# Kernel tuning notes

Hardware: AMD Instinct MI355X
Metric: run time of the kernel (lower is better)

The kernel has to match this reference:

```python
import jax, jax.numpy as jnp
import numpy as np

B, T, D, H, R = 64, 128, 128, 128, 4  # num_T == num_H == num_D forced by shape consistency
E = D * R  # SwiGLU expansion dim
EPS = 1e-5


def _pswiglu(x, Wu, bu, Wg, bg, Wd, bd):
    # x: [B,T,D]; per-token independent SwiGLU MLPs batched as one einsum
    up = jnp.einsum('btd,tde->bte', x, Wu) + bu          # [B,T,E]
    gate = jax.nn.silu(jnp.einsum('btd,tde->bte', x, Wg) + bg)
    return jnp.einsum('bte,ted->btd', up * gate, Wd) + bd  # [B,T,D]


def _rmsnorm(x, scale):
    rms = jnp.sqrt(jnp.mean(x * x, axis=-1, keepdims=True) + EPS)
    return x / rms * scale


def _token_mix(x, nT, nD, nH):
    # reshape (B,nT,nD)->(B,nT,nH,dk), transpose, merge -> (B,nH,nT*dk)
    dk = nD // nH
    b = x.shape[0]
    return x.reshape(b, nT, nH, dk).transpose(0, 2, 1, 3).reshape(b, nH, nT * dk)


def setup_inputs() -> dict:
    key = jax.random.key(0)
    ks = jax.random.split(key, 7)
    s = 0.02
    return {
        'x': jax.random.normal(ks[0], (B, T, D), dtype=jnp.float32),
        'W1_up': jax.random.normal(ks[1], (T, D, E), dtype=jnp.float32) * s,
        'b1_up': jnp.zeros((T, E), jnp.float32),
        'W1_gate': jax.random.normal(ks[2], (T, D, E), dtype=jnp.float32) * s,
        'b1_gate': jnp.zeros((T, E), jnp.float32),
        'W1_down': jax.random.normal(ks[3], (T, E, D), dtype=jnp.float32) * s,
        'b1_down': jnp.zeros((T, D), jnp.float32),
        'scale1': jnp.ones((D,), jnp.float32),
        'W2_up': jax.random.normal(ks[4], (T, D, E), dtype=jnp.float32) * s,
        'b2_up': jnp.zeros((T, E), jnp.float32),
        'W2_gate': jax.random.normal(ks[5], (T, D, E), dtype=jnp.float32) * s,
        'b2_gate': jnp.zeros((T, E), jnp.float32),
        'W2_down': jax.random.normal(ks[6], (T, E, D), dtype=jnp.float32) * s,
        'b2_down': jnp.zeros((T, D), jnp.float32),
        'scale2': jnp.ones((D,), jnp.float32),
    }


def reference(x, W1_up, b1_up, W1_gate, b1_gate, W1_down, b1_down, scale1,
              W2_up, b2_up, W2_gate, b2_gate, W2_down, b2_down, scale2):
    mixed = _token_mix(x, T, D, H)                         # [B,H,T*D/H] == [B,N,N]
    x1 = _rmsnorm(mixed + _pswiglu(mixed, W1_up, b1_up, W1_gate, b1_gate, W1_down, b1_down), scale1)
    rev = _token_mix(x1, T, H, D)                          # revert transpose
    out = _rmsnorm(rev + _pswiglu(rev, W2_up, b2_up, W2_gate, b2_gate, W2_down, b2_down), scale2)
    return out
```

## Files before the change

### kernel.cpp

```cpp
#include <hip/hip_runtime.h>

typedef __bf16 bf16x8 __attribute__((ext_vector_type(8)));
typedef float f32x4 __attribute__((ext_vector_type(4)));
typedef unsigned int uint;

union Frag { __bf16 b[8]; bf16x8 v; unsigned short u[8]; };

__device__ __forceinline__ unsigned short bfbits(float f) {
  union { __bf16 h; unsigned short s; } c; c.h = (__bf16)f; return c.s;
}
__device__ __forceinline__ float bf2f(unsigned short h) {
  return __uint_as_float(((uint)h) << 16);
}

#define BAR() asm volatile("s_waitcnt lgkmcnt(0)\n\ts_barrier" ::: "memory")

template <typename T>
__global__ __launch_bounds__(256) void transpose_in(const T* __restrict__ src,
                                                    unsigned short* __restrict__ dst) {
  __shared__ unsigned short tile[64][68];
  const int b  = blockIdx.x >> 2;
  const int f0 = ((blockIdx.x >> 1) & 1) * 64;
  const int s0 = (blockIdx.x & 1) * 64;
  const int j = threadIdx.x & 63, i0 = threadIdx.x >> 6;
  const T* sp = src + b * 16384 + f0 * 128 + s0 + j;
#pragma unroll
  for (int p = 0; p < 16; ++p) {
    const int i = i0 + p * 4;
    if constexpr (sizeof(T) == 4) tile[i][j] = bfbits((float)sp[i * 128]);
    else                          tile[i][j] = (unsigned short)sp[i * 128];
  }
  __syncthreads();
  unsigned short* dp = dst + s0 * 8192 + b * 128 + f0 + j;
#pragma unroll
  for (int p = 0; p < 16; ++p) {
    const int i = i0 + p * 4;
    dp[(size_t)i * 8192] = tile[j][i];
  }
}

__global__ __launch_bounds__(512, 4) void mlp_main(
    const unsigned short* __restrict__ Xt,
    const float* __restrict__ Wu, const float* __restrict__ bu,
    const float* __restrict__ Wg, const float* __restrict__ bg,
    const float* __restrict__ Wd,
    unsigned short* __restrict__ partial)
{
  const int bid = blockIdx.x;
  const int s = bid >> 2, q = bid & 3;
  const int tid = threadIdx.x;
  const int wv = tid >> 6, lane = tid & 63;
  const int l16 = lane & 15, lg = lane >> 4;
  const int col = wv * 16 + l16;

  __shared__ __align__(16) unsigned short xa[64 * 136];

  const float* WuS = Wu + (size_t)s * 65536 + q * 128;
  const float* WgS = Wg + (size_t)s * 65536 + q * 128;
  const float* WdS = Wd + (size_t)s * 65536 + (size_t)q * 16384;

  const float* pu = WuS + (size_t)(lg * 8) * 512 + col;
  const float* pg = WgS + (size_t)(lg * 8) * 512 + col;
  const float* pd = WdS + (size_t)(lg * 8) * 128 + col;

  float ub[2][8], gb[2][8], db[2][8];
#pragma unroll
  for (int j = 0; j < 8; ++j) { ub[0][j] = pu[(size_t)j * 512]; gb[0][j] = pg[(size_t)j * 512]; }
  const float buv = bu[s * 512 + q * 128 + col];
  const float bgv = bg[s * 512 + q * 128 + col];

#pragma unroll
  for (int cc = 0; cc < 2; ++cc) {
    const int c = tid * 2 + cc;
    const int m = c >> 4, ch = c & 15;
    uint4 v = *(const uint4*)(Xt + (size_t)s * 8192 + m * 128 + ch * 8);
    *(uint4*)&xa[m * 136 + ((ch ^ (m & 7)) << 3)] = v;
  }
  BAR();

  Frag a[4];
  f32x4 au[4] = {}, ag[4] = {};
#pragma unroll
  for (int kk = 0; kk < 4; ++kk) {
    if (kk < 3) {
#pragma unroll
      for (int j = 0; j < 8; ++j) {
        ub[(kk + 1) & 1][j] = pu[(size_t)((kk + 1) * 32 + j) * 512];
        gb[(kk + 1) & 1][j] = pg[(size_t)((kk + 1) * 32 + j) * 512];
      }
    }
#pragma unroll
    for (int mt = 0; mt < 4; ++mt) {
      const int m = mt * 16 + l16;
      a[mt].v = *(const bf16x8*)&xa[m * 136 + (((kk * 4 + lg) ^ (m & 7)) << 3)];
    }
    Frag fu, fg;
#pragma unroll
    for (int j = 0; j < 8; ++j) {
      fu.b[j] = (__bf16)ub[kk & 1][j];
      fg.b[j] = (__bf16)gb[kk & 1][j];
    }
#pragma unroll
    for (int mt = 0; mt < 4; ++mt) {
      au[mt] = __builtin_amdgcn_mfma_f32_16x16x32_bf16(a[mt].v, fu.v, au[mt], 0, 0, 0);
      ag[mt] = __builtin_amdgcn_mfma_f32_16x16x32_bf16(a[mt].v, fg.v, ag[mt], 0, 0, 0);
    }
  }

#pragma unroll
  for (int j = 0; j < 8; ++j) db[0][j] = pd[(size_t)j * 128];

  float a2v[4][4];
#pragma unroll
  for (int mt = 0; mt < 4; ++mt)
#pragma unroll
    for (int r = 0; r < 4; ++r) {
      const float uv = au[mt][r] + buv;
      const float gv = ag[mt][r] + bgv;
      a2v[mt][r] = uv * (gv / (1.f + __expf(-gv)));
    }

  BAR();
#pragma unroll
  for (int mt = 0; mt < 4; ++mt)
#pragma unroll
    for (int r = 0; r < 4; ++r) {
      const int m = mt * 16 + lg * 4 + r;
      xa[m * 136 + (((col >> 3) ^ (m & 7)) << 3) + (col & 7)] = bfbits(a2v[mt][r]);
    }
  BAR();

  f32x4 ad[4] = {};
#pragma unroll
  for (int kk = 0; kk < 4; ++kk) {
    if (kk < 3) {
#pragma unroll
      for (int j = 0; j < 8; ++j)
        db[(kk + 1) & 1][j] = pd[(size_t)((kk + 1) * 32 + j) * 128];
    }
#pragma unroll
    for (int mt = 0; mt < 4; ++mt) {
      const int m = mt * 16 + l16;
      a[mt].v = *(const bf16x8*)&xa[m * 136 + (((kk * 4 + lg) ^ (m & 7)) << 3)];
    }
    Frag fd;
#pragma unroll
    for (int j = 0; j < 8; ++j) fd.b[j] = (__bf16)db[kk & 1][j];
#pragma unroll
    for (int mt = 0; mt < 4; ++mt)
      ad[mt] = __builtin_amdgcn_mfma_f32_16x16x32_bf16(a[mt].v, fd.v, ad[mt], 0, 0, 0);
  }

  unsigned short* po = partial + (size_t)bid * 8192;
#pragma unroll
  for (int mt = 0; mt < 4; ++mt)
#pragma unroll
    for (int r = 0; r < 4; ++r)
      po[(mt * 16 + lg * 4 + r) * 128 + col] = bfbits(ad[mt][r]);
}

template <typename TO>
__global__ __launch_bounds__(256) void finish(
    const unsigned short* __restrict__ part, const unsigned short* __restrict__ xt,
    const float* __restrict__ bd, const float* __restrict__ scale,
    TO* __restrict__ y)
{
  const int s = blockIdx.x >> 1, half = blockIdx.x & 1;
  const int wvt = threadIdx.x >> 6, lane = threadIdx.x & 63;
  const int d0 = lane * 2;
  const float sc0 = scale[d0], sc1 = scale[d0 + 1];
  const float b0 = bd[s * 128 + d0], b1 = bd[s * 128 + d0 + 1];
  const unsigned short* pb = part + (size_t)s * 4 * 8192;
  const unsigned short* xb = xt + (size_t)s * 8192;
  for (int i = 0; i < 8; ++i) {
    const int b = half * 32 + i * 4 + wvt;
    const uint rx = *(const uint*)(xb + b * 128 + d0);
    float z0 = b0 + bf2f((unsigned short)rx);
    float z1 = b1 + bf2f((unsigned short)(rx >> 16));
#pragma unroll
    for (int p = 0; p < 4; ++p) {
      const uint rp = *(const uint*)(pb + p * 8192 + b * 128 + d0);
      z0 += bf2f((unsigned short)rp);
      z1 += bf2f((unsigned short)(rp >> 16));
    }
    float ss = z0 * z0 + z1 * z1;
#pragma unroll
    for (int off = 32; off; off >>= 1) ss += __shfl_xor(ss, off);
    const float inv = rsqrtf(ss * (1.f / 128.f) + 1e-5f);
    if constexpr (sizeof(TO) == 4) {
      float2 o = make_float2(z0 * inv * sc0, z1 * inv * sc1);
      *(float2*)((float*)y + (size_t)b * 16384 + s * 128 + d0) = o;
    } else {
      const uint o = (uint)bfbits(z0 * inv * sc0) | ((uint)bfbits(z1 * inv * sc1) << 16);
      *(uint*)((unsigned short*)y + (size_t)b * 16384 + s * 128 + d0) = o;
    }
  }
}

extern "C" void kernel_launch(void* const* d_in, const int* in_sizes, int n_in,
                              void* d_out, int out_size, void* d_ws, size_t ws_size,
                              hipStream_t stream) {
  (void)in_sizes; (void)n_in; (void)out_size; (void)ws_size;
  const float* x   = (const float*)d_in[0];
  const float* W1u = (const float*)d_in[1];
  const float* b1u = (const float*)d_in[2];
  const float* W1g = (const float*)d_in[3];
  const float* b1g = (const float*)d_in[4];
  const float* W1d = (const float*)d_in[5];
  const float* b1d = (const float*)d_in[6];
  const float* sc1 = (const float*)d_in[7];
  const float* W2u = (const float*)d_in[8];
  const float* b2u = (const float*)d_in[9];
  const float* W2g = (const float*)d_in[10];
  const float* b2g = (const float*)d_in[11];
  const float* W2d = (const float*)d_in[12];
  const float* b2d = (const float*)d_in[13];
  const float* sc2 = (const float*)d_in[14];
  float* out = (float*)d_out;

  unsigned short* xt   = (unsigned short*)d_ws;
  unsigned short* y1   = xt + (size_t)1048576;
  unsigned short* part = y1 + (size_t)1048576;

  transpose_in<float><<<256, 256, 0, stream>>>(x, xt);
  mlp_main<<<512, 512, 0, stream>>>(xt, W1u, b1u, W1g, b1g, W1d, part);
  finish<unsigned short><<<256, 256, 0, stream>>>(part, xt, b1d, sc1, y1);
  transpose_in<unsigned short><<<256, 256, 0, stream>>>(y1, xt);
  mlp_main<<<512, 512, 0, stream>>>(xt, W2u, b2u, W2g, b2g, W2d, part);
  finish<float><<<256, 256, 0, stream>>>(part, xt, b2d, sc2, out);
}
```

Measured before the change: 60.65 us.

## Stream weight tiles into LDS via async global_load_lds with triple buffering

Replaces per-thread register prefetch of fp32 weight columns with asynchronous global-to-LDS loads (global_load_lds) into a three-slot LDS ring buffer, keeping two weight tiles in flight while MFMAs consume the third. Barriers wait on vmcnt so loads overlap compute. The down-projection weights are prefetched during the gate/up phase. The activation tile drops its XOR swizzle in favour of a padded stride, and weight tiles get a column swizzle instead. This adds LDS use (about 48KB plus the activation tile), which may limit occupancy at 4 blocks per CU. It also adds more barriers.

```diff
diff --git a/kernel.cpp b/kernel.cpp
--- a/kernel.cpp
+++ b/kernel.cpp
@@ -4,6 +4,8 @@
 typedef float f32x4 __attribute__((ext_vector_type(4)));
 typedef unsigned int uint;
 
+#define XA_STR 152
+
 union Frag { __bf16 b[8]; bf16x8 v; unsigned short u[8]; };
 
 __device__ __forceinline__ unsigned short bfbits(float f) {
@@ -13,7 +15,8 @@
   return __uint_as_float(((uint)h) << 16);
 }
 
-#define BAR() asm volatile("s_waitcnt lgkmcnt(0)\n\ts_barrier" ::: "memory")
+#define WAIT_BAR(N) asm volatile("s_waitcnt vmcnt(" #N ") lgkmcnt(0)\n\ts_barrier" ::: "memory")
+#define LGKM_BAR()  asm volatile("s_waitcnt lgkmcnt(0)\n\ts_barrier" ::: "memory")
 
 template <typename T>
 __global__ __launch_bounds__(256) void transpose_in(const T* __restrict__ src,
@@ -53,62 +56,92 @@
   const int l16 = lane & 15, lg = lane >> 4;
   const int col = wv * 16 + l16;
 
-  __shared__ __align__(16) unsigned short xa[64 * 136];
+  __shared__ __align__(16) float wb[3][4096];
+  __shared__ __align__(16) unsigned short xa[64 * XA_STR];
 
   const float* WuS = Wu + (size_t)s * 65536 + q * 128;
   const float* WgS = Wg + (size_t)s * 65536 + q * 128;
   const float* WdS = Wd + (size_t)s * 65536 + (size_t)q * 16384;
 
-  const float* pu = WuS + (size_t)(lg * 8) * 512 + col;
-  const float* pg = WgS + (size_t)(lg * 8) * 512 + col;
-  const float* pd = WdS + (size_t)(lg * 8) * 128 + col;
-
-  float ub[2][8], gb[2][8], db[2][8];
-#pragma unroll
-  for (int j = 0; j < 8; ++j) { ub[0][j] = pu[(size_t)j * 512]; gb[0][j] = pg[(size_t)j * 512]; }
+  auto ISSUE = [&](const float* base, int rs, float* bb) {
+#pragma unroll
+    for (int r = 0; r < 2; ++r) {
+      const int p = (r << 9) + tid;
+      const int k = p >> 5, ch = p & 31;
+      const int chs = ch ^ (((k >> 3) & 1) << 2);
+      __builtin_amdgcn_global_load_lds(
+          (const __attribute__((address_space(1))) void*)(base + (size_t)k * rs + (chs << 2)),
+          (__attribute__((address_space(3))) void*)(bb + (p << 2)), 16, 0, 0);
+    }
+  };
+
+  Frag a[4];
+  auto LOADA = [&](int kk) {
+#pragma unroll
+    for (int mt = 0; mt < 4; ++mt)
+      a[mt].v = *(const bf16x8*)&xa[(mt * 16 + l16) * XA_STR + ((kk * 4 + lg) << 3)];
+  };
+
+  const int cswz = col ^ ((lg & 1) << 4);
+  auto BFRAG = [&](const float* bb) {
+    Frag f;
+    const float* bp = bb + (lg << 3) * 128 + cswz;
+#pragma unroll
+    for (int j = 0; j < 8; ++j) f.b[j] = (__bf16)bp[j * 128];
+    return f;
+  };
+
+  f32x4 au[4] = {}, ag[4] = {}, ad[4] = {};
+  auto MFMA4 = [&](const Frag& f, f32x4* acc) {
+#pragma unroll
+    for (int mt = 0; mt < 4; ++mt)
+      acc[mt] = __builtin_amdgcn_mfma_f32_16x16x32_bf16(a[mt].v, f.v, acc[mt], 0, 0, 0);
+  };
+
+  uint4 xv[2];
+#pragma unroll
+  for (int cc = 0; cc < 2; ++cc) {
+    const int p = (cc << 9) + tid;
+    const int m = p >> 4, ch = p & 15;
+    xv[cc] = *(const uint4*)(Xt + (size_t)s * 8192 + m * 128 + (ch << 3));
+  }
   const float buv = bu[s * 512 + q * 128 + col];
   const float bgv = bg[s * 512 + q * 128 + col];
-
+  __builtin_amdgcn_sched_barrier(0);
+  ISSUE(WuS, 512, wb[0]);
+  ISSUE(WgS, 512, wb[1]);
+  __builtin_amdgcn_sched_barrier(0);
 #pragma unroll
   for (int cc = 0; cc < 2; ++cc) {
-    const int c = tid * 2 + cc;
-    const int m = c >> 4, ch = c & 15;
-    uint4 v = *(const uint4*)(Xt + (size_t)s * 8192 + m * 128 + ch * 8);
-    *(uint4*)&xa[m * 136 + ((ch ^ (m & 7)) << 3)] = v;
-  }
-  BAR();
-
-  Frag a[4];
-  f32x4 au[4] = {}, ag[4] = {};
-#pragma unroll
-  for (int kk = 0; kk < 4; ++kk) {
-    if (kk < 3) {
-#pragma unroll
-      for (int j = 0; j < 8; ++j) {
-        ub[(kk + 1) & 1][j] = pu[(size_t)((kk + 1) * 32 + j) * 512];
-        gb[(kk + 1) & 1][j] = pg[(size_t)((kk + 1) * 32 + j) * 512];
-      }
-    }
-#pragma unroll
-    for (int mt = 0; mt < 4; ++mt) {
-      const int m = mt * 16 + l16;
-      a[mt].v = *(const bf16x8*)&xa[m * 136 + (((kk * 4 + lg) ^ (m & 7)) << 3)];
-    }
-    Frag fu, fg;
-#pragma unroll
-    for (int j = 0; j < 8; ++j) {
-      fu.b[j] = (__bf16)ub[kk & 1][j];
-      fg.b[j] = (__bf16)gb[kk & 1][j];
-    }
-#pragma unroll
-    for (int mt = 0; mt < 4; ++mt) {
-      au[mt] = __builtin_amdgcn_mfma_f32_16x16x32_bf16(a[mt].v, fu.v, au[mt], 0, 0, 0);
-      ag[mt] = __builtin_amdgcn_mfma_f32_16x16x32_bf16(a[mt].v, fg.v, ag[mt], 0, 0, 0);
-    }
-  }
-
-#pragma unroll
-  for (int j = 0; j < 8; ++j) db[0][j] = pd[(size_t)j * 128];
+    const int p = (cc << 9) + tid;
+    const int m = p >> 4, ch = p & 15;
+    *(uint4*)&xa[m * XA_STR + (ch << 3)] = xv[cc];
+  }
+
+  WAIT_BAR(2);
+  LOADA(0); { Frag f = BFRAG(wb[0]); MFMA4(f, au); }
+  ISSUE(WuS + 32 * 512, 512, wb[2]);
+  WAIT_BAR(2);
+  { Frag f = BFRAG(wb[1]); MFMA4(f, ag); }
+  ISSUE(WgS + 32 * 512, 512, wb[0]);
+  WAIT_BAR(2);
+  LOADA(1); { Frag f = BFRAG(wb[2]); MFMA4(f, au); }
+  ISSUE(WuS + 64 * 512, 512, wb[1]);
+  WAIT_BAR(2);
+  { Frag f = BFRAG(wb[0]); MFMA4(f, ag); }
+  ISSUE(WgS + 64 * 512, 512, wb[2]);
+  WAIT_BAR(2);
+  LOADA(2); { Frag f = BFRAG(wb[1]); MFMA4(f, au); }
+  ISSUE(WuS + 96 * 512, 512, wb[0]);
+  WAIT_BAR(2);
+  { Frag f = BFRAG(wb[2]); MFMA4(f, ag); }
+  ISSUE(WgS + 96 * 512, 512, wb[1]);
+  WAIT_BAR(2);
+  LOADA(3); { Frag f = BFRAG(wb[0]); MFMA4(f, au); }
+  ISSUE(WdS, 128, wb[2]);
+  WAIT_BAR(2);
+  { Frag f = BFRAG(wb[1]); MFMA4(f, ag); }
+  ISSUE(WdS + 32 * 128, 128, wb[0]);
 
   float a2v[4][4];
 #pragma unroll
@@ -119,37 +152,23 @@
       const float gv = ag[mt][r] + bgv;
       a2v[mt][r] = uv * (gv / (1.f + __expf(-gv)));
     }
-
-  BAR();
+  LGKM_BAR();
 #pragma unroll
   for (int mt = 0; mt < 4; ++mt)
 #pragma unroll
-    for (int r = 0; r < 4; ++r) {
-      const int m = mt * 16 + lg * 4 + r;
-      xa[m * 136 + (((col >> 3) ^ (m & 7)) << 3) + (col & 7)] = bfbits(a2v[mt][r]);
-    }
-  BAR();
-
-  f32x4 ad[4] = {};
-#pragma unroll
-  for (int kk = 0; kk < 4; ++kk) {
-    if (kk < 3) {
-#pragma unroll
-      for (int j = 0; j < 8; ++j)
-        db[(kk + 1) & 1][j] = pd[(size_t)((kk + 1) * 32 + j) * 128];
-    }
-#pragma unroll
-    for (int mt = 0; mt < 4; ++mt) {
-      const int m = mt * 16 + l16;
-      a[mt].v = *(const bf16x8*)&xa[m * 136 + (((kk * 4 + lg) ^ (m & 7)) << 3)];
-    }
-    Frag fd;
-#pragma unroll
-    for (int j = 0; j < 8; ++j) fd.b[j] = (__bf16)db[kk & 1][j];
-#pragma unroll
-    for (int mt = 0; mt < 4; ++mt)
-      ad[mt] = __builtin_amdgcn_mfma_f32_16x16x32_bf16(a[mt].v, fd.v, ad[mt], 0, 0, 0);
-  }
+    for (int r = 0; r < 4; ++r)
+      xa[(mt * 16 + lg * 4 + r) * XA_STR + col] = bfbits(a2v[mt][r]);
+
+  WAIT_BAR(2);
+  LOADA(0); { Frag f = BFRAG(wb[2]); MFMA4(f, ad); }
+  ISSUE(WdS + 64 * 128, 128, wb[1]);
+  WAIT_BAR(2);
+  LOADA(1); { Frag f = BFRAG(wb[0]); MFMA4(f, ad); }
+  ISSUE(WdS + 96 * 128, 128, wb[2]);
+  WAIT_BAR(2);
+  LOADA(2); { Frag f = BFRAG(wb[1]); MFMA4(f, ad); }
+  WAIT_BAR(0);
+  LOADA(3); { Frag f = BFRAG(wb[2]); MFMA4(f, ad); }
 
   unsigned short* po = partial + (size_t)bid * 8192;
 #pragma unroll
```

Result: slower. 61.88 us (+2.0%).

## Stage weights via vectorized inline-asm loads through LDS with deep prefetch

Applied to the files above, without the earlier changes.

Replaces the per-lane scalar strided weight loads in mlp_main with coalesced global_load_dwordx4 inline-asm loads that are staged through shared memory (SU/SG) and then read back transposed into bf16 fragments. Loads for up, gate and down weights are issued several k-steps ahead and tracked with explicit vmcnt waits, so down-projection weights stream in while the up/gate MFMAs run. The activation tile drops the XOR swizzle and uses a padded stride of 152 instead. Shared memory use grows and two barriers are added per k-step, which may reduce occupancy. The hand-counted vmcnt values are fragile if the compiler reorders or adds memory operations.

```diff
diff --git a/kernel.cpp b/kernel.cpp
--- a/kernel.cpp
+++ b/kernel.cpp
@@ -4,6 +4,8 @@
 typedef float f32x4 __attribute__((ext_vector_type(4)));
 typedef unsigned int uint;
 
+#define XA_STR 152
+
 union Frag { __bf16 b[8]; bf16x8 v; unsigned short u[8]; };
 
 __device__ __forceinline__ unsigned short bfbits(float f) {
@@ -13,7 +15,14 @@
   return __uint_as_float(((uint)h) << 16);
 }
 
-#define BAR() asm volatile("s_waitcnt lgkmcnt(0)\n\ts_barrier" ::: "memory")
+#define GLOAD4(dst, voff, base) \
+  asm volatile("global_load_dwordx4 %0, %1, %2" : "=v"(dst) : "v"(voff), "s"(base))
+#define GLOAD4I(dst, voff, base, IMM) \
+  asm volatile("global_load_dwordx4 %0, %1, %2 offset:" #IMM : "=v"(dst) : "v"(voff), "s"(base))
+#define GLOAD1(dst, voff, base) \
+  asm volatile("global_load_dword %0, %1, %2" : "=v"(dst) : "v"(voff), "s"(base))
+#define WAITV(N) asm volatile("s_waitcnt vmcnt(" #N ")" ::: "memory")
+#define BARX()   asm volatile("s_waitcnt lgkmcnt(0)\n\ts_barrier" ::: "memory")
 
 template <typename T>
 __global__ __launch_bounds__(256) void transpose_in(const T* __restrict__ src,
@@ -53,62 +62,86 @@
   const int l16 = lane & 15, lg = lane >> 4;
   const int col = wv * 16 + l16;
 
-  __shared__ __align__(16) unsigned short xa[64 * 136];
+  __shared__ __align__(16) float SU[32 * 128];
+  __shared__ __align__(16) float SG[32 * 128];
+  __shared__ __align__(16) unsigned short xa[64 * XA_STR];
 
   const float* WuS = Wu + (size_t)s * 65536 + q * 128;
   const float* WgS = Wg + (size_t)s * 65536 + q * 128;
   const float* WdS = Wd + (size_t)s * 65536 + (size_t)q * 16384;
-
-  const float* pu = WuS + (size_t)(lg * 8) * 512 + col;
-  const float* pg = WgS + (size_t)(lg * 8) * 512 + col;
-  const float* pd = WdS + (size_t)(lg * 8) * 128 + col;
-
-  float ub[2][8], gb[2][8], db[2][8];
-#pragma unroll
-  for (int j = 0; j < 8; ++j) { ub[0][j] = pu[(size_t)j * 512]; gb[0][j] = pg[(size_t)j * 512]; }
-  const float buv = bu[s * 512 + q * 128 + col];
-  const float bgv = bg[s * 512 + q * 128 + col];
-
-#pragma unroll
-  for (int cc = 0; cc < 2; ++cc) {
-    const int c = tid * 2 + cc;
-    const int m = c >> 4, ch = c & 15;
-    uint4 v = *(const uint4*)(Xt + (size_t)s * 8192 + m * 128 + ch * 8);
-    *(uint4*)&xa[m * 136 + ((ch ^ (m & 7)) << 3)] = v;
-  }
-  BAR();
+  const float* buS = bu + s * 512 + q * 128;
+  const float* bgS = bg + s * 512 + q * 128;
+  const unsigned short* XtS = Xt + (size_t)s * 8192;
+
+  uint vuo = (uint)((4 * wv + 2 + (lane >> 5)) * 2048 + (lane & 31) * 16);
+  uint vdo = (uint)((4 * wv + (lane >> 5)) * 512 + (lane & 31) * 16);
+  const uint vbo = (uint)(col * 4);
+  const uint vx0 = (uint)(tid * 16), vx1 = vx0 + 8192;
+
+  f32x4 uq[3][2], gq[3][2], dq[4][2];
+  f32x4 xq0, xq1;
+  float buv, bgv;
+
+#define ISSUE_U(SET) do { \
+    GLOAD4I(uq[SET][0], vuo, WuS, -4096); GLOAD4(uq[SET][1], vuo, WuS); \
+    GLOAD4I(gq[SET][0], vuo, WgS, -4096); GLOAD4(gq[SET][1], vuo, WgS); \
+    vuo += 65536; } while (0)
+#define ISSUE_D(SET) do { \
+    GLOAD4(dq[SET][0], vdo, WdS); GLOAD4I(dq[SET][1], vdo, WdS, 1024); \
+    vdo += 16384; } while (0)
+
+  GLOAD4(xq0, vx0, XtS);
+  GLOAD4(xq1, vx1, XtS);
+  GLOAD1(buv, vbo, buS);
+  GLOAD1(bgv, vbo, bgS);
+  ISSUE_U(0); ISSUE_U(1); ISSUE_U(2);
+
+  WAITV(12);
+  {
+    const int m0 = tid >> 4, ch0 = tid & 15;
+    *(f32x4*)&xa[m0 * XA_STR + (ch0 << 3)] = xq0;
+    const int p1 = tid + 512, m1 = p1 >> 4, ch1 = p1 & 15;
+    *(f32x4*)&xa[m1 * XA_STR + (ch1 << 3)] = xq1;
+  }
+  BARX();
+
+  const int wsA = (4 * wv + (lane >> 5)) * 128 + (lane & 31) * 4;
+  const int wsB = wsA + 256;
 
   Frag a[4];
-  f32x4 au[4] = {}, ag[4] = {};
-#pragma unroll
-  for (int kk = 0; kk < 4; ++kk) {
-    if (kk < 3) {
-#pragma unroll
-      for (int j = 0; j < 8; ++j) {
-        ub[(kk + 1) & 1][j] = pu[(size_t)((kk + 1) * 32 + j) * 512];
-        gb[(kk + 1) & 1][j] = pg[(size_t)((kk + 1) * 32 + j) * 512];
-      }
-    }
-#pragma unroll
-    for (int mt = 0; mt < 4; ++mt) {
-      const int m = mt * 16 + l16;
-      a[mt].v = *(const bf16x8*)&xa[m * 136 + (((kk * 4 + lg) ^ (m & 7)) << 3)];
-    }
-    Frag fu, fg;
-#pragma unroll
-    for (int j = 0; j < 8; ++j) {
-      fu.b[j] = (__bf16)ub[kk & 1][j];
-      fg.b[j] = (__bf16)gb[kk & 1][j];
-    }
-#pragma unroll
-    for (int mt = 0; mt < 4; ++mt) {
-      au[mt] = __builtin_amdgcn_mfma_f32_16x16x32_bf16(a[mt].v, fu.v, au[mt], 0, 0, 0);
-      ag[mt] = __builtin_amdgcn_mfma_f32_16x16x32_bf16(a[mt].v, fg.v, ag[mt], 0, 0, 0);
-    }
-  }
-
-#pragma unroll
-  for (int j = 0; j < 8; ++j) db[0][j] = pd[(size_t)j * 128];
+#define LOADA(KK) do { \
+    _Pragma("unroll") \
+    for (int mt = 0; mt < 4; ++mt) \
+      a[mt].v = *(const bf16x8*)&xa[(mt * 16 + l16) * XA_STR + (((KK) * 4 + lg) << 3)]; \
+  } while (0)
+
+#define BF(f, SL) do { \
+    const float* bp = (SL) + (lg * 8) * 128 + col; \
+    _Pragma("unroll") \
+    for (int j = 0; j < 8; ++j) f.b[j] = (__bf16)bp[j * 128]; } while (0)
+
+  f32x4 au[4] = {}, ag[4] = {}, ad[4] = {};
+#define MFMA4(f, acc) do { \
+    _Pragma("unroll") \
+    for (int mt = 0; mt < 4; ++mt) \
+      acc[mt] = __builtin_amdgcn_mfma_f32_16x16x32_bf16(a[mt].v, f.v, acc[mt], 0, 0, 0); \
+  } while (0)
+
+#define UP_STEP(SET, KK, ISSUE_STMT) do { \
+    BARX();  \
+    *(f32x4*)&SU[wsA] = uq[SET][0]; *(f32x4*)&SU[wsB] = uq[SET][1]; \
+    *(f32x4*)&SG[wsA] = gq[SET][0]; *(f32x4*)&SG[wsB] = gq[SET][1]; \
+    ISSUE_STMT; \
+    BARX();  \
+    LOADA(KK); \
+    { Frag fu; BF(fu, SU); MFMA4(fu, au); } \
+    { Frag fg; BF(fg, SG); MFMA4(fg, ag); } \
+  } while (0)
+
+  WAITV(8);  UP_STEP(0, 0, ISSUE_U(0));
+  WAITV(8);  UP_STEP(1, 1, ISSUE_D(0));
+  WAITV(6);  UP_STEP(2, 2, ISSUE_D(1));
+  WAITV(4);  UP_STEP(0, 3, ISSUE_D(2));
 
   float a2v[4][4];
 #pragma unroll
@@ -119,37 +152,26 @@
       const float gv = ag[mt][r] + bgv;
       a2v[mt][r] = uv * (gv / (1.f + __expf(-gv)));
     }
-
-  BAR();
+  BARX();
 #pragma unroll
   for (int mt = 0; mt < 4; ++mt)
 #pragma unroll
-    for (int r = 0; r < 4; ++r) {
-      const int m = mt * 16 + lg * 4 + r;
-      xa[m * 136 + (((col >> 3) ^ (m & 7)) << 3) + (col & 7)] = bfbits(a2v[mt][r]);
-    }
-  BAR();
-
-  f32x4 ad[4] = {};
-#pragma unroll
-  for (int kk = 0; kk < 4; ++kk) {
-    if (kk < 3) {
-#pragma unroll
-      for (int j = 0; j < 8; ++j)
-        db[(kk + 1) & 1][j] = pd[(size_t)((kk + 1) * 32 + j) * 128];
-    }
-#pragma unroll
-    for (int mt = 0; mt < 4; ++mt) {
-      const int m = mt * 16 + l16;
-      a[mt].v = *(const bf16x8*)&xa[m * 136 + (((kk * 4 + lg) ^ (m & 7)) << 3)];
-    }
-    Frag fd;
-#pragma unroll
-    for (int j = 0; j < 8; ++j) fd.b[j] = (__bf16)db[kk & 1][j];
-#pragma unroll
-    for (int mt = 0; mt < 4; ++mt)
-      ad[mt] = __builtin_amdgcn_mfma_f32_16x16x32_bf16(a[mt].v, fd.v, ad[mt], 0, 0, 0);
-  }
+    for (int r = 0; r < 4; ++r)
+      xa[(mt * 16 + lg * 4 + r) * XA_STR + col] = bfbits(a2v[mt][r]);
+  ISSUE_D(3);
+
+#define DN_STEP(SET, KK) do { \
+    BARX(); \
+    *(f32x4*)&SU[wsA] = dq[SET][0]; *(f32x4*)&SU[wsB] = dq[SET][1]; \
+    BARX(); \
+    LOADA(KK); \
+    { Frag fd; BF(fd, SU); MFMA4(fd, ad); } \
+  } while (0)
+
+  WAITV(6);  DN_STEP(0, 0);
+  WAITV(4);  DN_STEP(1, 1);
+  WAITV(2);  DN_STEP(2, 2);
+  WAITV(0);  DN_STEP(3, 3);
 
   unsigned short* po = partial + (size_t)bid * 8192;
 #pragma unroll
@@ -157,6 +179,14 @@
 #pragma unroll
     for (int r = 0; r < 4; ++r)
       po[(mt * 16 + lg * 4 + r) * 128 + col] = bfbits(ad[mt][r]);
+
+#undef ISSUE_U
+#undef ISSUE_D
+#undef LOADA
+#undef BF
+#undef MFMA4
+#undef UP_STEP
+#undef DN_STEP
 }
 
 template <typename TO>
```

Measured after the change: 66.73 us. +10.0%, slower.
